# Performance work log

Hardware: AMD Instinct MI355X
Metric: run time of the kernel (lower is better)

The kernel has to match this reference:

```python
import jax, jax.numpy as jnp
import numpy as np

NUM_EXPERTS = 8
TOP_K = 2
P_NORM = 1.0  # moe_normalize_expert_weights
HIDDEN = 1024
FFN_HIDDEN = 2048
BATCH, SEQ = 2, 2048


def setup_inputs() -> dict:
    key = jax.random.key(0)
    ks = jax.random.split(key, 5)
    s = 0.02
    return {
        "x": jax.random.normal(ks[0], (BATCH, SEQ, HIDDEN), dtype=jnp.float32),
        "router_w": jax.random.normal(ks[1], (NUM_EXPERTS, HIDDEN), dtype=jnp.float32) * s,
        "w1": jax.random.normal(ks[2], (NUM_EXPERTS, FFN_HIDDEN, HIDDEN), dtype=jnp.float32) * s,
        "v1": jax.random.normal(ks[3], (NUM_EXPERTS, FFN_HIDDEN, HIDDEN), dtype=jnp.float32) * s,
        "w2": jax.random.normal(ks[4], (NUM_EXPERTS, FFN_HIDDEN, HIDDEN), dtype=jnp.float32) * s,
    }


def reference(x, router_w, w1, v1, w2):
    B, S, H = x.shape
    xf = x.reshape(-1, H)  # [T, H]

    # Router: softmax in fp32, top-k, L-p normalize, cast back.
    logits = xf @ router_w.T  # [T, E]
    probs = jax.nn.softmax(logits.astype(jnp.float32), axis=-1)
    top_w, top_e = jax.lax.top_k(probs, TOP_K)  # [T, K]
    norm = jnp.sum(jnp.abs(top_w) ** P_NORM, axis=-1, keepdims=True) ** (1.0 / P_NORM)
    top_w = (top_w / norm).astype(x.dtype)

    # Per-token combine weight for each expert: c[t,e] = sum_k top_w[t,k]*[top_e[t,k]==e]
    c = jnp.sum(jax.nn.one_hot(top_e, NUM_EXPERTS, dtype=x.dtype) * top_w[..., None], axis=1)  # [T, E]

    # Dense per-expert GLU; routing realized by output gating with c (zero for unrouted tokens).
    out = jnp.zeros_like(xf)
    for e in range(NUM_EXPERTS):
        h = jax.nn.silu(xf @ w1[e].T) * (xf @ v1[e].T)  # [T, F]
        out = out + (h @ w2[e]) * c[:, e:e + 1]  # [T, H]
    return out.reshape(B, S, H)
```

## Files before the change

### kernel.cpp

```cpp
#include <hip/hip_runtime.h>
#include <stdint.h>

#define T_TOKENS 4096
#define HID 1024
#define FFN 2048
#define NE 8

typedef __attribute__((ext_vector_type(8))) short bf16x8;
typedef __attribute__((ext_vector_type(4))) float f32x4;

__device__ __forceinline__ unsigned short f2bf(float f) {
  union { float f; uint32_t u; } v; v.f = f;
  uint32_t r = v.u + 0x7FFFu + ((v.u >> 16) & 1u);
  return (unsigned short)(r >> 16);
}

__device__ __forceinline__ uint32_t pack2(float a, float b) {
  return (uint32_t)f2bf(a) | ((uint32_t)f2bf(b) << 16);
}

__device__ __forceinline__ void gload16(const unsigned short* g, unsigned short* l) {
  __builtin_amdgcn_global_load_lds(
      (const __attribute__((address_space(1))) void*)(g),
      (__attribute__((address_space(3))) void*)(l), 16, 0, 0);
}

__device__ __forceinline__ int frag_off(int r, int g) {
  return r * 32 + ((g ^ ((r >> 1) & 3)) << 3);
}

constexpr size_t XBF_OFF  = 0;
constexpr size_t HBUF_OFF = (size_t)T_TOKENS * HID * 2;
constexpr size_t TOKE_OFF = HBUF_OFF + (size_t)T_TOKENS * 2 * FFN * 2;
constexpr size_t TOKW_OFF = TOKE_OFF + (size_t)T_TOKENS * 2 * 4;
constexpr size_t CNT_OFF  = TOKW_OFF + (size_t)T_TOKENS * 2 * 4;
constexpr size_t OFF_OFF  = CNT_OFF + 64;
constexpr size_t LIST_OFF = OFF_OFF + 64;
constexpr size_t META_END = LIST_OFF + (size_t)NE * T_TOKENS * 4;
constexpr size_t PB1_OFF  = META_END;
constexpr size_t PB2_OFF  = PB1_OFF + (size_t)NE * FFN * HID * 2;
constexpr size_t PW2_OFF  = PB2_OFF + (size_t)NE * FFN * HID * 2;
constexpr size_t WS_BIG   = PW2_OFF + (size_t)NE * HID * FFN * 2;
constexpr size_t YBUF_OFF = PB1_OFF;

__global__ __launch_bounds__(256) void pack_w1v1_kernel(const float* __restrict__ w1,
                                                        const float* __restrict__ v1,
                                                        unsigned short* __restrict__ pb1,
                                                        unsigned short* __restrict__ pb2) {
  int colblk = blockIdx.x;
  int kslab  = blockIdx.y;
  int ez     = blockIdx.z;
  const float* src = (ez < NE) ? w1 : v1;
  unsigned short* dst = (ez < NE) ? pb1 : pb2;
  int e = ez & (NE - 1);
  __shared__ unsigned short lds[2048];
  int t = threadIdx.x;
  int c  = colblk * 16 + (t >> 4);
  int k0 = kslab * 128 + (t & 15) * 8;
  const float* sp = src + ((size_t)e * FFN + c) * HID + k0;
  float4 a = *(const float4*)sp;
  float4 b = *(const float4*)(sp + 4);
  uint4 o;
  o.x = pack2(a.x, a.y); o.y = pack2(a.z, a.w);
  o.z = pack2(b.x, b.y); o.w = pack2(b.z, b.w);
  int chunk = ((t & 15) >> 2) * 64 + ((t & 3) * 16 + (t >> 4));
  int pos = chunk ^ ((chunk >> 4) & 15);
  *(uint4*)(lds + pos * 8) = o;
  __syncthreads();
  int rpos = t ^ ((t >> 4) & 15);
  uint4 v = *(const uint4*)(lds + rpos * 8);
  unsigned short* dp = dst + (((size_t)e * (FFN / 16) + colblk) * (HID / 32) + kslab * 4) * 512 + t * 8;
  *(uint4*)dp = v;
}

__global__ __launch_bounds__(256) void pack_w2_kernel(const float* __restrict__ w2,
                                                      unsigned short* __restrict__ pw2) {
  int cb = blockIdx.x;
  int kb = blockIdx.y;
  int e  = blockIdx.z;
  __shared__ unsigned short s[64][68];
  int t = threadIdx.x;
  int tr = t >> 4, tc = (t & 15) * 4;
  const float* src = w2 + ((size_t)e * FFN + kb * 64) * HID + cb * 64;
#pragma unroll
  for (int i = 0; i < 4; ++i) {
    int k = tr + i * 16;
    float4 v = *(const float4*)(src + (size_t)k * HID + tc);
    s[k][tc + 0] = f2bf(v.x); s[k][tc + 1] = f2bf(v.y);
    s[k][tc + 2] = f2bf(v.z); s[k][tc + 3] = f2bf(v.w);
  }
  __syncthreads();
#pragma unroll
  for (int half = 0; half < 2; ++half) {
    int cid = t + half * 256;
    int colblk_l = cid >> 7;
    int ks_l = (cid >> 6) & 1;
    int lane = cid & 63;
    unsigned short tmp[8];
#pragma unroll
    for (int j = 0; j < 8; ++j)
      tmp[j] = s[ks_l * 32 + (lane >> 4) * 8 + j][colblk_l * 16 + (lane & 15)];
    uint4 o;
    o.x = tmp[0] | (tmp[1] << 16); o.y = tmp[2] | (tmp[3] << 16);
    o.z = tmp[4] | (tmp[5] << 16); o.w = tmp[6] | (tmp[7] << 16);
    unsigned short* dp = pw2 + (((size_t)e * (HID / 16) + cb * 4 + colblk_l) * (FFN / 32)
                                + kb * 2 + ks_l) * 512 + lane * 8;
    *(uint4*)dp = o;
  }
}

__global__ __launch_bounds__(256) void router_kernel(const float* __restrict__ x,
                                                     const float* __restrict__ rw,
                                                     int* __restrict__ tok_e,
                                                     float* __restrict__ tok_w,
                                                     unsigned short* __restrict__ xbf) {
  __shared__ float s_rw[NE * HID];
  int tid = threadIdx.x;
  for (int i = tid; i < NE * HID / 4; i += 256)
    ((float4*)s_rw)[i] = ((const float4*)rw)[i];
  __syncthreads();
  int wave = tid >> 6, lane = tid & 63;
  int t = blockIdx.x * 4 + wave;
  const float* xr = x + (size_t)t * HID;
  unsigned short* xbr = xbf + (size_t)t * HID;
  float acc[NE];
#pragma unroll
  for (int e = 0; e < NE; ++e) acc[e] = 0.0f;
  for (int c = 0; c < HID / 64; ++c) {
    int idx = c * 64 + lane;
    float xv = xr[idx];
    xbr[idx] = f2bf(xv);
#pragma unroll
    for (int e = 0; e < NE; ++e) acc[e] += xv * s_rw[e * HID + idx];
  }
#pragma unroll
  for (int e = 0; e < NE; ++e)
    for (int off = 32; off > 0; off >>= 1) acc[e] += __shfl_down(acc[e], off);
  if (lane == 0) {
    float m = acc[0];
#pragma unroll
    for (int e = 1; e < NE; ++e) m = fmaxf(m, acc[e]);
    float p[NE], Z = 0.0f;
#pragma unroll
    for (int e = 0; e < NE; ++e) { p[e] = expf(acc[e] - m); Z += p[e]; }
    int e0 = 0;
#pragma unroll
    for (int e = 1; e < NE; ++e) if (p[e] > p[e0]) e0 = e;
    int e1 = (e0 == 0) ? 1 : 0;
#pragma unroll
    for (int e = 0; e < NE; ++e) if (e != e0 && p[e] > p[e1]) e1 = e;
    float w0 = p[e0] / Z, w1 = p[e1] / Z;
    float nrm = w0 + w1;
    tok_e[t * 2] = e0; tok_e[t * 2 + 1] = e1;
    tok_w[t * 2] = w0 / nrm; tok_w[t * 2 + 1] = w1 / nrm;
  }
}

__global__ __launch_bounds__(1024) void scatter_offsets_kernel(
    const int* __restrict__ tok_e, int* __restrict__ counts,
    int* __restrict__ offs, int* __restrict__ lists) {
  __shared__ int c[NE];
  int tid = threadIdx.x;
  if (tid < NE) c[tid] = 0;
  __syncthreads();
  for (int p = tid; p < T_TOKENS * 2; p += 1024) {
    int e = tok_e[p];
    int pos = atomicAdd(&c[e], 1);
    lists[e * T_TOKENS + pos] = p;
  }
  __syncthreads();
  if (tid == 0) {
    int r = 0;
    for (int e = 0; e < NE; ++e) { counts[e] = c[e]; offs[e] = r; r += c[e]; }
  }
}

__global__ __launch_bounds__(256) void combine_kernel(const float* __restrict__ ybuf,
                                                      float* __restrict__ out) {
  int t = blockIdx.x;
  int c = threadIdx.x;
  const float4* y0 = (const float4*)(ybuf + (size_t)(2 * t) * HID);
  const float4* y1 = (const float4*)(ybuf + (size_t)(2 * t + 1) * HID);
  float4 a = y0[c], b = y1[c];
  float4 r; r.x = a.x + b.x; r.y = a.y + b.y; r.z = a.z + b.z; r.w = a.w + b.w;
  ((float4*)(out + (size_t)t * HID))[c] = r;
}

__global__ __launch_bounds__(512) void gemm1b_kernel(
    const unsigned short* __restrict__ xbf,
    const unsigned short* __restrict__ pb1, const unsigned short* __restrict__ pb2,
    const int* __restrict__ counts, const int* __restrict__ offs,
    const int* __restrict__ lists, unsigned short* __restrict__ hbuf) {
  constexpr int ABUF = 128 * 32;
  constexpr int BBUF = 128 * 32;
  constexpr int NT = HID / 32;
  int nt = blockIdx.x, mt = blockIdx.y, e = blockIdx.z;
  int ne = counts[e];
  if (mt * 128 >= ne) return;
  __shared__ unsigned short s_a[2 * ABUF];
  __shared__ unsigned short s_b1[2 * BBUF];
  int tid = threadIdx.x;
  int srow = tid >> 2, slot = tid & 3;
  int lchunk = slot ^ ((srow >> 1) & 3);
  const int* lst = lists + e * T_TOKENS + mt * 128;
  int tok = lst[(mt * 128 + srow < ne) ? srow : 0] >> 1;
  const unsigned short* aptr = xbf + (size_t)tok * HID + lchunk * 8;
  int g8 = tid >> 6, ln = tid & 63;
  const unsigned short* b1p =
      pb1 + ((size_t)(e * (FFN / 16) + nt * 8 + g8) * (HID / 32)) * 512 + ln * 8;

  int lane = tid & 63, wv = tid >> 6;
  int wm = (wv >> 2) * 64, wn = (wv & 3) * 32;
  int rl = lane & 15, g = lane >> 4;
  int aoff[4];
#pragma unroll
  for (int m = 0; m < 4; ++m) aoff[m] = frag_off(wm + m * 16 + rl, g);
  int b1off[2];
#pragma unroll
  for (int n = 0; n < 2; ++n) b1off[n] = (((wv & 3) * 2 + n) * 64 + lane) * 8;
  size_t cb2 = (size_t)e * (FFN / 16) + nt * 8 + (wv & 3) * 2;
  const unsigned short* p2_0 = pb2 + (cb2 + 0) * (HID / 32) * 512 + lane * 8;
  const unsigned short* p2_1 = pb2 + (cb2 + 1) * (HID / 32) * 512 + lane * 8;

  f32x4 zero = {0.0f, 0.0f, 0.0f, 0.0f};
  f32x4 acc1[4][2], acc2[4][2];
#pragma unroll
  for (int i = 0; i < 4; ++i)
#pragma unroll
    for (int j = 0; j < 2; ++j) { acc1[i][j] = zero; acc2[i][j] = zero; }

  auto stage = [&](int s, int t) {
    gload16(aptr + t * 32, s_a + s * ABUF + tid * 8);
    gload16(b1p + (size_t)t * 512, s_b1 + s * BBUF + tid * 8);
  };
  bf16x8 b2X[2], b2Y[2];
  auto loadBX = [&](int t) {
    b2X[0] = *(const bf16x8*)(p2_0 + (size_t)t * 512);
    b2X[1] = *(const bf16x8*)(p2_1 + (size_t)t * 512);
  };
  auto loadBY = [&](int t) {
    b2Y[0] = *(const bf16x8*)(p2_0 + (size_t)t * 512);
    b2Y[1] = *(const bf16x8*)(p2_1 + (size_t)t * 512);
  };
  auto compute = [&](int s, bf16x8 (&b2)[2]) {
    const unsigned short* pa = s_a + s * ABUF;
    const unsigned short* pb = s_b1 + s * BBUF;
    bf16x8 af[4], bf1[2];
#pragma unroll
    for (int m = 0; m < 4; ++m) af[m] = *(const bf16x8*)(pa + aoff[m]);
#pragma unroll
    for (int n = 0; n < 2; ++n) bf1[n] = *(const bf16x8*)(pb + b1off[n]);
#pragma unroll
    for (int m = 0; m < 4; ++m)
#pragma unroll
      for (int n = 0; n < 2; ++n) {
        acc1[m][n] = __builtin_amdgcn_mfma_f32_16x16x32_bf16(af[m], bf1[n], acc1[m][n], 0, 0, 0);
        acc2[m][n] = __builtin_amdgcn_mfma_f32_16x16x32_bf16(af[m], b2[n], acc2[m][n], 0, 0, 0);
      }
  };

  stage(0, 0);
  loadBX(0);
  __syncthreads();
  for (int t = 0; t < NT; t += 2) {
    stage(1, t + 1);
    loadBY(t + 1);
    compute(0, b2X);
    __syncthreads();
    if (t + 2 < NT) { stage(0, t + 2); loadBX(t + 2); }
    compute(1, b2Y);
    __syncthreads();
  }

  int hb = offs[e];
#pragma unroll
  for (int m = 0; m < 4; ++m) {
#pragma unroll
    for (int j = 0; j < 4; ++j) {
      int r = mt * 128 + wm + m * 16 + (lane >> 4) * 4 + j;
      if (r < ne) {
        size_t rowo = (size_t)(hb + r) * FFN;
#pragma unroll
        for (int n = 0; n < 2; ++n) {
          int col = nt * 128 + wn + n * 16 + rl;
          float c1 = acc1[m][n][j], c2 = acc2[m][n][j];
          float h = c1 / (1.0f + __expf(-c1)) * c2;
          hbuf[rowo + col] = f2bf(h);
        }
      }
    }
  }
}

__global__ __launch_bounds__(512) void gemm2b_kernel(
    const unsigned short* __restrict__ hbuf, const unsigned short* __restrict__ pw2,
    const int* __restrict__ counts, const int* __restrict__ offs,
    const int* __restrict__ lists, const float* __restrict__ tok_w,
    float* __restrict__ ybuf) {
  constexpr int BUFSZ = 128 * 32;
  constexpr int NT = FFN / 32;
  int nt = blockIdx.x, mt = blockIdx.y, e = blockIdx.z;
  int ne = counts[e];
  if (mt * 128 >= ne) return;
  __shared__ unsigned short s_a[2 * BUFSZ];
  int tid = threadIdx.x;
  int hb = offs[e];
  int srow = tid >> 2, slot = tid & 3;
  int lchunk = slot ^ ((srow >> 1) & 3);
  int ar = mt * 128 + ((mt * 128 + srow < ne) ? srow : 0);
  const unsigned short* aptr = hbuf + (size_t)(hb + ar) * FFN + lchunk * 8;

  int lane = tid & 63, wv = tid >> 6;
  int wm = (wv >> 2) * 64, wn = (wv & 3) * 32;
  int rl = lane & 15, g = lane >> 4;
  int aoff[4];
#pragma unroll
  for (int m = 0; m < 4; ++m) aoff[m] = frag_off(wm + m * 16 + rl, g);

  size_t cb = (size_t)e * (HID / 16) + nt * 8 + (wv & 3) * 2;
  const unsigned short* p_0 = pw2 + (cb + 0) * (FFN / 32) * 512 + lane * 8;
  const unsigned short* p_1 = pw2 + (cb + 1) * (FFN / 32) * 512 + lane * 8;

  f32x4 zero = {0.0f, 0.0f, 0.0f, 0.0f};
  f32x4 acc[4][2];
#pragma unroll
  for (int i = 0; i < 4; ++i)
#pragma unroll
    for (int j = 0; j < 2; ++j) acc[i][j] = zero;

  auto stageA = [&](int s, int t) {
    gload16(aptr + t * 32, s_a + s * BUFSZ + tid * 8);
  };
  bf16x8 bX[2], bY[2];
  auto loadBX = [&](int t) {
    bX[0] = *(const bf16x8*)(p_0 + (size_t)t * 512);
    bX[1] = *(const bf16x8*)(p_1 + (size_t)t * 512);
  };
  auto loadBY = [&](int t) {
    bY[0] = *(const bf16x8*)(p_0 + (size_t)t * 512);
    bY[1] = *(const bf16x8*)(p_1 + (size_t)t * 512);
  };
  auto compute = [&](int s, bf16x8 (&b)[2]) {
    const unsigned short* pa = s_a + s * BUFSZ;
    bf16x8 af[4];
#pragma unroll
    for (int m = 0; m < 4; ++m) af[m] = *(const bf16x8*)(pa + aoff[m]);
#pragma unroll
    for (int m = 0; m < 4; ++m)
#pragma unroll
      for (int n = 0; n < 2; ++n)
        acc[m][n] = __builtin_amdgcn_mfma_f32_16x16x32_bf16(af[m], b[n], acc[m][n], 0, 0, 0);
  };

  stageA(0, 0);
  loadBX(0);
  __syncthreads();
  for (int t = 0; t < NT; t += 2) {
    stageA(1, t + 1);
    loadBY(t + 1);
    compute(0, bX);
    __syncthreads();
    if (t + 2 < NT) { stageA(0, t + 2); loadBX(t + 2); }
    compute(1, bY);
    __syncthreads();
  }

#pragma unroll
  for (int m = 0; m < 4; ++m) {
#pragma unroll
    for (int j = 0; j < 4; ++j) {
      int r = mt * 128 + wm + m * 16 + (lane >> 4) * 4 + j;
      if (r < ne) {
        int p = lists[e * T_TOKENS + r];
        float w = tok_w[p];
        float* yrow = ybuf + (size_t)p * HID;
#pragma unroll
        for (int n = 0; n < 2; ++n) {
          int col = nt * 128 + wn + n * 16 + rl;
          yrow[col] = acc[m][n][j] * w;
        }
      }
    }
  }
}


__global__ __launch_bounds__(512) void gemm1_kernel(
    const unsigned short* __restrict__ xbf,
    const float* __restrict__ w1, const float* __restrict__ v1,
    const int* __restrict__ counts, const int* __restrict__ offs,
    const int* __restrict__ lists, unsigned short* __restrict__ hbuf) {
  int nt = blockIdx.x, mt = blockIdx.y, e = blockIdx.z;
  int ne = counts[e];
  if (mt * 128 >= ne) return;
  int nrows = ne - mt * 128; if (nrows > 128) nrows = 128;
  __shared__ unsigned short s_a[128 * 40];
  __shared__ unsigned short s_b1[128 * 40];
  __shared__ unsigned short s_b2[128 * 40];
  const int* lst = lists + e * T_TOKENS + mt * 128;
  int tid = threadIdx.x;
  int sr = tid >> 2, sc = tid & 3;
  int pr = lst[(sr < nrows) ? sr : 0];
  const unsigned short* asrc = xbf + (size_t)(pr >> 1) * HID + sc * 8;
  size_t brow = ((size_t)e * FFN + nt * 128 + sr) * HID + sc * 8;
  const float* b1s = w1 + brow;
  const float* b2s = v1 + brow;
  int lane = tid & 63, wv = tid >> 6;
  int wm = (wv >> 2) * 64, wn = (wv & 3) * 32;
  int rl = lane & 15, kg = (lane >> 4) * 8;
  f32x4 zero = {0.0f, 0.0f, 0.0f, 0.0f};
  f32x4 acc1[4][2], acc2[4][2];
#pragma unroll
  for (int i = 0; i < 4; ++i)
#pragma unroll
    for (int j = 0; j < 2; ++j) { acc1[i][j] = zero; acc2[i][j] = zero; }
  int sdst = sr * 40 + sc * 8;
  for (int kk = 0; kk < HID; kk += 32) {
    uint4 av = *(const uint4*)(asrc + kk);
    float4 f0 = *(const float4*)(b1s + kk);
    float4 f1 = *(const float4*)(b1s + kk + 4);
    float4 g0 = *(const float4*)(b2s + kk);
    float4 g1 = *(const float4*)(b2s + kk + 4);
    *(uint4*)(s_a + sdst) = av;
    uint4 bv; bv.x = pack2(f0.x, f0.y); bv.y = pack2(f0.z, f0.w);
    bv.z = pack2(f1.x, f1.y); bv.w = pack2(f1.z, f1.w);
    *(uint4*)(s_b1 + sdst) = bv;
    uint4 cv; cv.x = pack2(g0.x, g0.y); cv.y = pack2(g0.z, g0.w);
    cv.z = pack2(g1.x, g1.y); cv.w = pack2(g1.z, g1.w);
    *(uint4*)(s_b2 + sdst) = cv;
    __syncthreads();
    bf16x8 af[4], bf1[2], bf2[2];
#pragma unroll
    for (int m = 0; m < 4; ++m)
      af[m] = *(const bf16x8*)(s_a + (wm + m * 16 + rl) * 40 + kg);
#pragma unroll
    for (int n = 0; n < 2; ++n) {
      bf1[n] = *(const bf16x8*)(s_b1 + (wn + n * 16 + rl) * 40 + kg);
      bf2[n] = *(const bf16x8*)(s_b2 + (wn + n * 16 + rl) * 40 + kg);
    }
#pragma unroll
    for (int m = 0; m < 4; ++m)
#pragma unroll
      for (int n = 0; n < 2; ++n) {
        acc1[m][n] = __builtin_amdgcn_mfma_f32_16x16x32_bf16(af[m], bf1[n], acc1[m][n], 0, 0, 0);
        acc2[m][n] = __builtin_amdgcn_mfma_f32_16x16x32_bf16(af[m], bf2[n], acc2[m][n], 0, 0, 0);
      }
    __syncthreads();
  }
  int hb = offs[e];
#pragma unroll
  for (int m = 0; m < 4; ++m) {
#pragma unroll
    for (int j = 0; j < 4; ++j) {
      int r = mt * 128 + wm + m * 16 + (lane >> 4) * 4 + j;
      if (r < ne) {
        size_t rowo = (size_t)(hb + r) * FFN;
#pragma unroll
        for (int n = 0; n < 2; ++n) {
          int col = nt * 128 + wn + n * 16 + rl;
          float c1 = acc1[m][n][j], c2 = acc2[m][n][j];
          float h = c1 / (1.0f + __expf(-c1)) * c2;
          hbuf[rowo + col] = f2bf(h);
        }
      }
    }
  }
}

__global__ __launch_bounds__(512) void gemm2_kernel(
    const unsigned short* __restrict__ hbuf, const float* __restrict__ w2,
    const int* __restrict__ counts, const int* __restrict__ offs,
    const int* __restrict__ lists, const float* __restrict__ tok_w,
    float* __restrict__ out) {
  int nt = blockIdx.x, mt = blockIdx.y, e = blockIdx.z;
  int ne = counts[e];
  if (mt * 128 >= ne) return;
  int nrows = ne - mt * 128; if (nrows > 128) nrows = 128;
  __shared__ unsigned short s_a[128 * 40];
  __shared__ unsigned short s_b[128 * 40];
  int tid = threadIdx.x;
  int hb = offs[e];
  int sr = tid >> 2, sc = tid & 3;
  int ar = mt * 128 + ((sr < nrows) ? sr : 0);
  const unsigned short* asrc = hbuf + (size_t)(hb + ar) * FFN + sc * 8;
  int bk = tid >> 4, bn = tid & 15;
  const float* bsrc = w2 + ((size_t)e * FFN + bk) * HID + nt * 128 + bn;
  int lane = tid & 63, wv = tid >> 6;
  int wm = (wv >> 2) * 64, wn = (wv & 3) * 32;
  int rl = lane & 15, kg = (lane >> 4) * 8;
  f32x4 zero = {0.0f, 0.0f, 0.0f, 0.0f};
  f32x4 acc[4][2];
#pragma unroll
  for (int i = 0; i < 4; ++i)
#pragma unroll
    for (int j = 0; j < 2; ++j) acc[i][j] = zero;
  int sdst = sr * 40 + sc * 8;
  for (int kk = 0; kk < FFN; kk += 32) {
    uint4 av = *(const uint4*)(asrc + kk);
    const float* bs = bsrc + (size_t)kk * HID;
    float bvals[8];
#pragma unroll
    for (int i = 0; i < 8; ++i) bvals[i] = bs[i * 16];
    *(uint4*)(s_a + sdst) = av;
#pragma unroll
    for (int i = 0; i < 8; ++i) s_b[(bn + i * 16) * 40 + bk] = f2bf(bvals[i]);
    __syncthreads();
    bf16x8 af[4], bfr[2];
#pragma unroll
    for (int m = 0; m < 4; ++m)
      af[m] = *(const bf16x8*)(s_a + (wm + m * 16 + rl) * 40 + kg);
#pragma unroll
    for (int n = 0; n < 2; ++n)
      bfr[n] = *(const bf16x8*)(s_b + (wn + n * 16 + rl) * 40 + kg);
#pragma unroll
    for (int m = 0; m < 4; ++m)
#pragma unroll
      for (int n = 0; n < 2; ++n)
        acc[m][n] = __builtin_amdgcn_mfma_f32_16x16x32_bf16(af[m], bfr[n], acc[m][n], 0, 0, 0);
    __syncthreads();
  }
#pragma unroll
  for (int m = 0; m < 4; ++m) {
#pragma unroll
    for (int j = 0; j < 4; ++j) {
      int r = mt * 128 + wm + m * 16 + (lane >> 4) * 4 + j;
      if (r < ne) {
        int p = lists[e * T_TOKENS + r];
        float w = tok_w[p];
        float* orow = out + (size_t)(p >> 1) * HID;
#pragma unroll
        for (int n = 0; n < 2; ++n) {
          int col = nt * 128 + wn + n * 16 + rl;
          atomicAdd(orow + col, acc[m][n][j] * w);
        }
      }
    }
  }
}

extern "C" void kernel_launch(void* const* d_in, const int* in_sizes, int n_in,
                              void* d_out, int out_size, void* d_ws, size_t ws_size,
                              hipStream_t stream) {
  const float* x  = (const float*)d_in[0];
  const float* rw = (const float*)d_in[1];
  const float* w1 = (const float*)d_in[2];
  const float* v1 = (const float*)d_in[3];
  const float* w2 = (const float*)d_in[4];
  float* out = (float*)d_out;
  char* ws = (char*)d_ws;
  if (ws_size < META_END) return;

  unsigned short* xbf  = (unsigned short*)(ws + XBF_OFF);
  unsigned short* hbuf = (unsigned short*)(ws + HBUF_OFF);
  int*   tok_e  = (int*)(ws + TOKE_OFF);
  float* tok_w  = (float*)(ws + TOKW_OFF);
  int*   counts = (int*)(ws + CNT_OFF);
  int*   offs   = (int*)(ws + OFF_OFF);
  int*   lists  = (int*)(ws + LIST_OFF);

  router_kernel<<<T_TOKENS / 4, 256, 0, stream>>>(x, rw, tok_e, tok_w, xbf);
  scatter_offsets_kernel<<<1, 1024, 0, stream>>>(tok_e, counts, offs, lists);

  if (ws_size >= WS_BIG) {
    unsigned short* pb1 = (unsigned short*)(ws + PB1_OFF);
    unsigned short* pb2 = (unsigned short*)(ws + PB2_OFF);
    unsigned short* pw2 = (unsigned short*)(ws + PW2_OFF);
    float* ybuf = (float*)(ws + YBUF_OFF);
    pack_w1v1_kernel<<<dim3(FFN / 16, HID / 128, 2 * NE), 256, 0, stream>>>(w1, v1, pb1, pb2);
    pack_w2_kernel<<<dim3(HID / 64, FFN / 64, NE), 256, 0, stream>>>(w2, pw2);
    gemm1b_kernel<<<dim3(FFN / 128, T_TOKENS / 128, NE), 512, 0, stream>>>(
        xbf, pb1, pb2, counts, offs, lists, hbuf);
    gemm2b_kernel<<<dim3(HID / 128, T_TOKENS / 128, NE), 512, 0, stream>>>(
        hbuf, pw2, counts, offs, lists, tok_w, ybuf);
    combine_kernel<<<T_TOKENS, 256, 0, stream>>>(ybuf, out);
  } else {
    hipMemsetAsync(d_out, 0, (size_t)T_TOKENS * HID * 4, stream);
    gemm1_kernel<<<dim3(FFN / 128, T_TOKENS / 128, NE), 512, 0, stream>>>(
        xbf, w1, v1, counts, offs, lists, hbuf);
    gemm2_kernel<<<dim3(HID / 128, T_TOKENS / 128, NE), 512, 0, stream>>>(
        hbuf, w2, counts, offs, lists, tok_w, out);
  }
}
```

Before: 255.8 us.

## Triple-buffer gemm1b loads with explicit vmcnt waits and MFMA priority

Changes the gemm1b main loop from double buffering to a three-stage LDS and register pipeline, so each tile is prefetched three iterations ahead. It replaces __syncthreads with hand-written s_waitcnt vmcnt plus s_barrier, waiting only on the oldest outstanding loads. It also raises wave priority around the MFMA block with s_setprio. The goal is to hide more global-load latency. The cost is more LDS and more registers, and the hand-counted vmcnt values are fragile, since NT=32 is not a multiple of 3 and needs the two-tile tail.

Result: slower. 280.3 us (+9.6%).

```diff
diff --git a/kernel.cpp b/kernel.cpp
--- a/kernel.cpp
+++ b/kernel.cpp
@@ -197,8 +197,8 @@
   int nt = blockIdx.x, mt = blockIdx.y, e = blockIdx.z;
   int ne = counts[e];
   if (mt * 128 >= ne) return;
-  __shared__ unsigned short s_a[2 * ABUF];
-  __shared__ unsigned short s_b1[2 * BBUF];
+  __shared__ unsigned short s_a[3 * ABUF];
+  __shared__ unsigned short s_b1[3 * BBUF];
   int tid = threadIdx.x;
   int srow = tid >> 2, slot = tid & 3;
   int lchunk = slot ^ ((srow >> 1) & 3);
@@ -233,16 +233,11 @@
     gload16(aptr + t * 32, s_a + s * ABUF + tid * 8);
     gload16(b1p + (size_t)t * 512, s_b1 + s * BBUF + tid * 8);
   };
-  bf16x8 b2X[2], b2Y[2];
-  auto loadBX = [&](int t) {
-    b2X[0] = *(const bf16x8*)(p2_0 + (size_t)t * 512);
-    b2X[1] = *(const bf16x8*)(p2_1 + (size_t)t * 512);
-  };
-  auto loadBY = [&](int t) {
-    b2Y[0] = *(const bf16x8*)(p2_0 + (size_t)t * 512);
-    b2Y[1] = *(const bf16x8*)(p2_1 + (size_t)t * 512);
-  };
-  auto compute = [&](int s, bf16x8 (&b2)[2]) {
+  auto loadB2 = [&](bf16x8 (&d)[2], int t) {
+    d[0] = *(const bf16x8*)(p2_0 + (size_t)t * 512);
+    d[1] = *(const bf16x8*)(p2_1 + (size_t)t * 512);
+  };
+  auto compute = [&](int s, const bf16x8 (&b2)[2]) {
     const unsigned short* pa = s_a + s * ABUF;
     const unsigned short* pb = s_b1 + s * BBUF;
     bf16x8 af[4], bf1[2];
@@ -250,6 +245,7 @@
     for (int m = 0; m < 4; ++m) af[m] = *(const bf16x8*)(pa + aoff[m]);
 #pragma unroll
     for (int n = 0; n < 2; ++n) bf1[n] = *(const bf16x8*)(pb + b1off[n]);
+    __builtin_amdgcn_s_setprio(1);
 #pragma unroll
     for (int m = 0; m < 4; ++m)
 #pragma unroll
@@ -257,20 +253,30 @@
         acc1[m][n] = __builtin_amdgcn_mfma_f32_16x16x32_bf16(af[m], bf1[n], acc1[m][n], 0, 0, 0);
         acc2[m][n] = __builtin_amdgcn_mfma_f32_16x16x32_bf16(af[m], b2[n], acc2[m][n], 0, 0, 0);
       }
-  };
-
-  stage(0, 0);
-  loadBX(0);
-  __syncthreads();
-  for (int t = 0; t < NT; t += 2) {
-    stage(1, t + 1);
-    loadBY(t + 1);
-    compute(0, b2X);
-    __syncthreads();
-    if (t + 2 < NT) { stage(0, t + 2); loadBX(t + 2); }
-    compute(1, b2Y);
-    __syncthreads();
-  }
+    __builtin_amdgcn_s_setprio(0);
+  };
+
+  bf16x8 b2a[2], b2b[2], b2c[2];
+  stage(0, 0); loadB2(b2a, 0);
+  stage(1, 1); loadB2(b2b, 1);
+  stage(2, 2); loadB2(b2c, 2);
+
+#define G1_ITER(S, B2, T, WAIT)                                               \
+  asm volatile("s_waitcnt vmcnt(" #WAIT ")\n\ts_barrier" ::: "memory");       \
+  compute(S, B2);                                                             \
+  asm volatile("s_barrier" ::: "memory");                                     \
+  if ((T) + 3 < NT) { stage(S, (T) + 3); loadB2(B2, (T) + 3); }
+
+  for (int t = 0; t < NT - 2; t += 3) {
+    G1_ITER(0, b2a, t, 8)
+    G1_ITER(1, b2b, t + 1, 8)
+    G1_ITER(2, b2c, t + 2, 8)
+  }
+  asm volatile("s_waitcnt vmcnt(4)\n\ts_barrier" ::: "memory");
+  compute(0, b2a);
+  asm volatile("s_waitcnt vmcnt(0)\n\ts_barrier" ::: "memory");
+  compute(1, b2b);
+#undef G1_ITER
 
   int hb = offs[e];
 #pragma unroll
```
